# Kernel optimization log

Hardware: AMD Instinct MI355X
Metric: run time of the kernel (lower is better)

Reference implementation:

```python
import jax, jax.numpy as jnp
import numpy as np

N_NODES = 50000
N_EDGES = 800000
F_IN = 128
HID = 128  # hidden_dim * num_heads with num_heads=1
N_GRAPHS = 32
N_LAYERS = 4
NEG_SLOPE = 0.2
LN_EPS = 1e-5


def setup_inputs() -> dict:
    key = jax.random.key(0)
    ks = jax.random.split(key, 20)
    x = jax.random.normal(ks[0], (N_NODES, F_IN), dtype=jnp.float32)
    edge_index = jax.random.randint(ks[1], (2, N_EDGES), 0, N_NODES, dtype=jnp.int32)
    batch = jnp.sort(jax.random.randint(ks[2], (N_NODES,), 0, N_GRAPHS, dtype=jnp.int32))
    s = 0.05
    Ws = jax.random.normal(ks[3], (N_LAYERS, F_IN, HID), dtype=jnp.float32) * s
    a_src = jax.random.normal(ks[4], (N_LAYERS, HID), dtype=jnp.float32) * s
    a_dst = jax.random.normal(ks[5], (N_LAYERS, HID), dtype=jnp.float32) * s
    gat_b = jnp.zeros((N_LAYERS, HID), dtype=jnp.float32)
    ln_g = jnp.ones((N_LAYERS, HID), dtype=jnp.float32)
    ln_b = jnp.zeros((N_LAYERS, HID), dtype=jnp.float32)
    skip_W = jax.random.normal(ks[6], (F_IN, HID), dtype=jnp.float32) * s
    skip_b = jnp.zeros((HID,), dtype=jnp.float32)
    W1 = jax.random.normal(ks[7], (2 * HID, HID), dtype=jnp.float32) * s
    b1 = jnp.zeros((HID,), dtype=jnp.float32)
    W2 = jax.random.normal(ks[8], (HID, HID // 2), dtype=jnp.float32) * s
    b2 = jnp.zeros((HID // 2,), dtype=jnp.float32)
    W3 = jax.random.normal(ks[9], (HID // 2, 4), dtype=jnp.float32) * s
    b3 = jnp.zeros((4,), dtype=jnp.float32)
    return dict(x=x, edge_index=edge_index, batch=batch, Ws=Ws, a_src=a_src,
                a_dst=a_dst, gat_b=gat_b, ln_g=ln_g, ln_b=ln_b,
                skip_W=skip_W, skip_b=skip_b, W1=W1, b1=b1, W2=W2, b2=b2, W3=W3, b3=b3)


def _gat_layer(x, W, a_s, a_d, b, src, dst, n_nodes):
    # linear transform (single head)
    h = x @ W                                  # [N, C]
    e_src = h @ a_s                            # [N]
    e_dst = h @ a_d                            # [N]
    e = jax.nn.leaky_relu(e_src[src] + e_dst[dst], NEG_SLOPE)  # [E']
    # segment softmax over destination nodes
    m = jax.ops.segment_max(e, dst, num_segments=n_nodes)      # [N]
    p = jnp.exp(e - m[dst])
    z = jax.ops.segment_sum(p, dst, num_segments=n_nodes)      # [N]
    alpha = p / z[dst]                                         # [E']
    out = jax.ops.segment_sum(h[src] * alpha[:, None], dst, num_segments=n_nodes)
    return out + b


def _layernorm(x, g, b):
    mu = jnp.mean(x, axis=-1, keepdims=True)
    var = jnp.var(x, axis=-1, keepdims=True)
    return (x - mu) * jax.lax.rsqrt(var + LN_EPS) * g + b


def reference(x, edge_index, batch, Ws, a_src, a_dst, gat_b, ln_g, ln_b,
              skip_W, skip_b, W1, b1, W2, b2, W3, b3):
    n = x.shape[0]
    # PyG GATConv default: add self loops
    loops = jnp.arange(n, dtype=edge_index.dtype)
    src = jnp.concatenate([edge_index[0], loops])
    dst = jnp.concatenate([edge_index[1], loops])

    skip = x @ skip_W + skip_b
    h = x
    for i in range(N_LAYERS):
        h_new = _gat_layer(h, Ws[i], a_src[i], a_dst[i], gat_b[i], src, dst, n)
        h_new = _layernorm(h_new, ln_g[i], ln_b[i])
        if i < N_LAYERS - 1:
            h_new = jax.nn.elu(h_new)
        h = h_new + (skip if i == 0 else h)
    # global mean + max pool over graphs
    bidx = batch
    cnt = jax.ops.segment_sum(jnp.ones((n,), h.dtype), bidx, num_segments=N_GRAPHS)
    x_mean = jax.ops.segment_sum(h, bidx, num_segments=N_GRAPHS) / jnp.maximum(cnt, 1.0)[:, None]
    x_max = jax.ops.segment_max(h, bidx, num_segments=N_GRAPHS)
    g = jnp.concatenate([x_mean, x_max], axis=1)           # [G, 2*HID]
    g = jax.nn.relu(g @ W1 + b1)
    g = jax.nn.relu(g @ W2 + b2)
    return g @ W3 + b3
```

## Files before the change

### kernel.cpp

```cpp
#include <hip/hip_runtime.h>
#include <hip/hip_fp16.h>
#include <math.h>

#define NND 50000
#define NE  800000
#define HID 128
#define NGR 32
#define NLAYER 4
#define NPL 8
#define TOT8 (NND * NPL)
#define KSLOT 16

typedef _Float16 half8 __attribute__((ext_vector_type(8)));
typedef float float4v __attribute__((ext_vector_type(4)));

static __device__ __forceinline__ unsigned fenc(float f){
  unsigned u = __float_as_uint(f);
  return (u & 0x80000000u) ? ~u : (u | 0x80000000u);
}
static __device__ __forceinline__ float fdec(unsigned u){
  return __uint_as_float((u & 0x80000000u) ? (u & 0x7fffffffu) : ~u);
}

__global__ __launch_bounds__(256) void k_prep(const float* __restrict__ Ws, const float* __restrict__ skip_W,
    _Float16* __restrict__ wth, const int* __restrict__ ei, int* __restrict__ cnt8p,
    unsigned short* __restrict__ csrf, int E, int N)
{
  if (blockIdx.x < 5) {
    int m = blockIdx.x;
    const float* src = (m < 4) ? (Ws + (size_t)m * 16384) : skip_W;
    _Float16* oh = wth + (size_t)m * 16384;
    for (int i = threadIdx.x; i < 16384; i += 256){
      int c = i >> 7, k = i & 127;
      oh[i] = (_Float16)src[k * 128 + c];
    }
    return;
  }
  int base = (blockIdx.x - 5) * 1024 + threadIdx.x;
  int p = blockIdx.x & 7;
  int srcs[4]; int cells[4]; bool val[4];
#pragma unroll
  for (int i = 0; i < 4; ++i) {
    int e = base + i * 256;
    val[i] = e < E + N;
    int s = 0, d = 0;
    if (val[i]) {
      if (e < E) { s = ei[e]; d = ei[E + e]; } else { s = e - E; d = e - E; }
    }
    srcs[i] = s; cells[i] = p * NND + d;
  }
  int r[4];
#pragma unroll
  for (int i = 0; i < 4; ++i) r[i] = val[i] ? atomicAdd(&cnt8p[cells[i]], 1) : KSLOT;
#pragma unroll
  for (int i = 0; i < 4; ++i)
    if (r[i] < KSLOT) csrf[(size_t)cells[i] * KSLOT + r[i]] = (unsigned short)srcs[i];
}

static __device__ __forceinline__ void gemm_body(int row0, const float* __restrict__ A,
    const _Float16* __restrict__ wt, const float* __restrict__ bias,
    const float* __restrict__ a_s, const float* __restrict__ a_d,
    float* __restrict__ outF, _Float16* __restrict__ outH,
    float* __restrict__ es, float* __restrict__ ed, int N)
{
  int tid = threadIdx.x;
  int w  = tid >> 6;
  int l  = tid & 63;
  int ln = l & 15;
  int q  = l >> 4;

  int row = row0 + w * 16 + ln;
  bool rok = row < N;
  const float4* Arow = (const float4*)(A + (size_t)(rok ? row : 0) * 128);

  half8 af[4];
#pragma unroll
  for (int k32 = 0; k32 < 4; ++k32) {
    int f4 = k32 * 8 + q * 2;
    float4 a0 = make_float4(0.f,0.f,0.f,0.f), a1 = a0;
    if (rok) { a0 = Arow[f4]; a1 = Arow[f4 + 1]; }
    half8 h = {(_Float16)a0.x, (_Float16)a0.y, (_Float16)a0.z, (_Float16)a0.w,
               (_Float16)a1.x, (_Float16)a1.y, (_Float16)a1.z, (_Float16)a1.w};
    af[k32] = h;
  }

  float4v acc[8];
#pragma unroll
  for (int t = 0; t < 8; ++t) acc[t] = (float4v){0.f, 0.f, 0.f, 0.f};

#pragma unroll
  for (int k32 = 0; k32 < 4; ++k32) {
    int kk = k32 * 32 + q * 8;
#pragma unroll
    for (int t = 0; t < 8; ++t) {
      half8 bv = *(const half8*)(&wt[(size_t)(t * 16 + ln) * 128 + kk]);
      acc[t] = __builtin_amdgcn_mfma_f32_16x16x32_f16(af[k32], bv, acc[t], 0, 0, 0);
    }
  }

  float bb[8];
  if (bias) {
#pragma unroll
    for (int t = 0; t < 8; ++t) bb[t] = bias[t * 16 + ln];
  }
#pragma unroll
  for (int t = 0; t < 8; ++t) {
#pragma unroll
    for (int r = 0; r < 4; ++r) {
      int gr = row0 + w * 16 + q * 4 + r;
      if (gr < N) {
        int col = t * 16 + ln;
        float v = acc[t][r] + (bias ? bb[t] : 0.f);
        if (outF) outF[(size_t)gr * 128 + col] = v;
        if (outH) outH[(size_t)gr * 128 + col] = (_Float16)v;
      }
    }
  }
  if (a_s) {
    float asv[8], adv[8];
#pragma unroll
    for (int t = 0; t < 8; ++t) { asv[t] = a_s[t * 16 + ln]; adv[t] = a_d[t * 16 + ln]; }
    float ps[4], pd[4];
#pragma unroll
    for (int r = 0; r < 4; ++r) {
      float s_ = 0.f, d_ = 0.f;
#pragma unroll
      for (int t = 0; t < 8; ++t) { s_ += acc[t][r] * asv[t]; d_ += acc[t][r] * adv[t]; }
      ps[r] = s_; pd[r] = d_;
    }
#pragma unroll
    for (int o = 1; o < 16; o <<= 1) {
#pragma unroll
      for (int r = 0; r < 4; ++r) { ps[r] += __shfl_xor(ps[r], o); pd[r] += __shfl_xor(pd[r], o); }
    }
    if (ln == 0) {
#pragma unroll
      for (int r = 0; r < 4; ++r) {
        int gr = row0 + w * 16 + q * 4 + r;
        if (gr < N) { es[gr] = ps[r]; ed[gr] = pd[r]; }
      }
    }
  }
}

__global__ __launch_bounds__(256) void gemm_mfma(const float* __restrict__ A,
    const _Float16* __restrict__ wt, const float* __restrict__ bias,
    const float* __restrict__ a_s, const float* __restrict__ a_d,
    float* __restrict__ outF, _Float16* __restrict__ outH,
    float* __restrict__ es, float* __restrict__ ed, int N)
{
  gemm_body(blockIdx.x * 64, A, wt, bias, a_s, a_d, outF, outH, es, ed, N);
}

__global__ __launch_bounds__(256) void k_gemm0_tr(const float* __restrict__ x,
    const _Float16* __restrict__ wt, const float* __restrict__ a_s, const float* __restrict__ a_d,
    _Float16* __restrict__ hW, float* __restrict__ es, float* __restrict__ ed,
    int gblocks, const int* __restrict__ cnt8p, int* __restrict__ cnt8d, int N)
{
  if ((int)blockIdx.x < gblocks) {
    gemm_body(blockIdx.x * 64, x, wt, nullptr, a_s, a_d, nullptr, hW, es, ed, N);
    return;
  }
  int d = (blockIdx.x - gblocks) * 256 + threadIdx.x;
  if (d >= NND) return;
  int c[8];
#pragma unroll
  for (int k = 0; k < 8; ++k) c[k] = cnt8p[k * NND + d];
  ((int4*)(cnt8d + (size_t)d * NPL))[0] = make_int4(c[0], c[1], c[2], c[3]);
  ((int4*)(cnt8d + (size_t)d * NPL))[1] = make_int4(c[4], c[5], c[6], c[7]);
}

__global__ __launch_bounds__(256) void edge_agg(
    const __half* __restrict__ hW, const float* __restrict__ es, const float* __restrict__ ed,
    const int* __restrict__ cnt8d, const unsigned short* __restrict__ csrf,
    const float* __restrict__ gb, const float* __restrict__ lg, const float* __restrict__ lb,
    const float* __restrict__ resid, float* __restrict__ hout, int do_elu, int N)
{
  __shared__ uint2 s_as[4][64];
  int wid = threadIdx.x >> 6;
  int lane = threadIdx.x & 63;
  int sub = lane >> 4;
  int sl  = lane & 15;
  int dst = blockIdx.x * 4 + wid;
  if (dst >= N) return;

  uint4 cA = ((const uint4*)(cnt8d + (size_t)dst * NPL))[0];
  uint4 cB = ((const uint4*)(cnt8d + (size_t)dst * NPL))[1];
  int cntv[8] = {(int)cA.x,(int)cA.y,(int)cA.z,(int)cA.w,(int)cB.x,(int)cB.y,(int)cB.z,(int)cB.w};
  int cum[9]; cum[0] = 0;
#pragma unroll
  for (int k = 0; k < 8; ++k) cum[k + 1] = cum[k] + cntv[k];
  int deg = cum[8];
  float edv = ed[dst];

  float acc[8];
#pragma unroll
  for (int k = 0; k < 8; ++k) acc[k] = 0.f;
  const uint4* h4 = (const uint4*)hW;
  const unsigned short* cbase = csrf + (size_t)dst * KSLOT;

  if (deg <= 64) {
    int s = 0;
    if (lane < deg) {
      int p = 0;
#pragma unroll
      for (int k = 1; k < 8; ++k) if (lane >= cum[k]) p = k;
      int er = lane - cum[p]; er = er < KSLOT ? er : (KSLOT - 1);
      s = cbase[(size_t)p * (NND * KSLOT) + er];
    }
    const int PF = 4;
    uint4 qd_pre[PF];
#pragma unroll
    for (int i = 0; i < PF; ++i) {
      int idx = (i << 2) | sub;
      int sv = __shfl(s, idx);
      qd_pre[i] = make_uint4(0u, 0u, 0u, 0u);
      if (idx < deg) qd_pre[i] = h4[(size_t)sv * 16 + sl];
    }
    float x = -1e30f;
    if (lane < deg) {
      float xx = es[s] + edv;
      x = xx > 0.f ? xx : 0.2f * xx;
    }
    float m = x;
#pragma unroll
    for (int o = 32; o; o >>= 1) m = fmaxf(m, __shfl_xor(m, o));
    float p_ = (lane < deg) ? __expf(x - m) : 0.f;
    float z = p_;
#pragma unroll
    for (int o = 32; o; o >>= 1) z += __shfl_xor(z, o);
    float a_l = p_ / z;

    int iters = (deg + 3) >> 2;
#pragma unroll
    for (int i = 0; i < PF; ++i) {
      int idx = (i << 2) | sub;
      float a = __shfl(a_l, idx);
      uint4 qd = qd_pre[i];
      float2 f0 = __half22float2(*(__half2*)&qd.x);
      float2 f1 = __half22float2(*(__half2*)&qd.y);
      float2 f2 = __half22float2(*(__half2*)&qd.z);
      float2 f3 = __half22float2(*(__half2*)&qd.w);
      acc[0] += a * f0.x; acc[1] += a * f0.y;
      acc[2] += a * f1.x; acc[3] += a * f1.y;
      acc[4] += a * f2.x; acc[5] += a * f2.y;
      acc[6] += a * f3.x; acc[7] += a * f3.y;
    }
    for (int i = PF; i < iters; ++i) {
      int idx = (i << 2) | sub;
      float a = __shfl(a_l, idx);
      int sv = __shfl(s, idx);
      if (idx < deg) {
        uint4 qd = h4[(size_t)sv * 16 + sl];
        float2 f0 = __half22float2(*(__half2*)&qd.x);
        float2 f1 = __half22float2(*(__half2*)&qd.y);
        float2 f2 = __half22float2(*(__half2*)&qd.z);
        float2 f3 = __half22float2(*(__half2*)&qd.w);
        acc[0] += a * f0.x; acc[1] += a * f0.y;
        acc[2] += a * f1.x; acc[3] += a * f1.y;
        acc[4] += a * f2.x; acc[5] += a * f2.y;
        acc[6] += a * f3.x; acc[7] += a * f3.y;
      }
    }
  } else {
    float m = -1e30f;
    for (int j = lane; j < deg; j += 64) {
      int p = 0;
#pragma unroll
      for (int k = 1; k < 8; ++k) if (j >= cum[k]) p = k;
      int er = j - cum[p]; er = er < KSLOT ? er : (KSLOT - 1);
      float x = es[cbase[(size_t)p * (NND * KSLOT) + er]] + edv;
      x = x > 0.f ? x : 0.2f * x;
      m = fmaxf(m, x);
    }
#pragma unroll
    for (int o = 32; o; o >>= 1) m = fmaxf(m, __shfl_xor(m, o));
    float z = 0.f;
    for (int j = lane; j < deg; j += 64) {
      int p = 0;
#pragma unroll
      for (int k = 1; k < 8; ++k) if (j >= cum[k]) p = k;
      int er = j - cum[p]; er = er < KSLOT ? er : (KSLOT - 1);
      float x = es[cbase[(size_t)p * (NND * KSLOT) + er]] + edv;
      x = x > 0.f ? x : 0.2f * x;
      z += __expf(x - m);
    }
#pragma unroll
    for (int o = 32; o; o >>= 1) z += __shfl_xor(z, o);
    float inv_z = 1.0f / z;
    for (int c0 = 0; c0 < deg; c0 += 64) {
      int j = c0 + lane;
      int cnt = min(64, deg - c0);
      int s = 0; float p_ = 0.f;
      if (j < deg) {
        int p = 0;
#pragma unroll
        for (int k = 1; k < 8; ++k) if (j >= cum[k]) p = k;
        int er = j - cum[p]; er = er < KSLOT ? er : (KSLOT - 1);
        s = cbase[(size_t)p * (NND * KSLOT) + er];
        float x = es[s] + edv;
        x = x > 0.f ? x : 0.2f * x;
        p_ = __expf(x - m) * inv_z;
      }
      s_as[wid][lane] = make_uint2(__float_as_uint(p_), (unsigned)s);
      int iters = (cnt + 3) >> 2;
      for (int i = 0; i < iters; ++i) {
        int idx = (i << 2) | sub;
        bool valid = idx < cnt;
        uint2 av = s_as[wid][valid ? idx : 0];
        float a = valid ? __uint_as_float(av.x) : 0.f;
        uint4 qd = h4[(size_t)av.y * 16 + sl];
        float2 f0 = __half22float2(*(__half2*)&qd.x);
        float2 f1 = __half22float2(*(__half2*)&qd.y);
        float2 f2 = __half22float2(*(__half2*)&qd.z);
        float2 f3 = __half22float2(*(__half2*)&qd.w);
        acc[0] += a * f0.x; acc[1] += a * f0.y;
        acc[2] += a * f1.x; acc[3] += a * f1.y;
        acc[4] += a * f2.x; acc[5] += a * f2.y;
        acc[6] += a * f3.x; acc[7] += a * f3.y;
      }
    }
  }

#pragma unroll
  for (int k = 0; k < 8; ++k) {
    acc[k] += __shfl_xor(acc[k], 16);
    acc[k] += __shfl_xor(acc[k], 32);
  }

  float4 g0 = ((const float4*)gb)[sl * 2];
  float4 g1 = ((const float4*)gb)[sl * 2 + 1];
  float v[8];
  v[0] = acc[0] + g0.x; v[1] = acc[1] + g0.y; v[2] = acc[2] + g0.z; v[3] = acc[3] + g0.w;
  v[4] = acc[4] + g1.x; v[5] = acc[5] + g1.y; v[6] = acc[6] + g1.z; v[7] = acc[7] + g1.w;
  float s1 = 0.f, s2 = 0.f;
#pragma unroll
  for (int k = 0; k < 8; ++k) { s1 += v[k]; s2 += v[k] * v[k]; }
#pragma unroll
  for (int o = 8; o; o >>= 1) { s1 += __shfl_xor(s1, o); s2 += __shfl_xor(s2, o); }
  float mu = s1 * (1.f / 128.f);
  float var = s2 * (1.f / 128.f) - mu * mu;
  float rstd = rsqrtf(var + 1e-5f);

  float va = sub == 0 ? v[0] : (sub == 1 ? v[2] : (sub == 2 ? v[4] : v[6]));
  float vb = sub == 0 ? v[1] : (sub == 1 ? v[3] : (sub == 2 ? v[5] : v[7]));
  int col = sl * 8 + sub * 2;
  float2 Lv = *(const float2*)(lg + col);
  float2 Bv = *(const float2*)(lb + col);
  float2 Rv = *(const float2*)(resid + (long)dst * 128 + col);
  float t0 = (va - mu) * rstd * Lv.x + Bv.x;
  float t1 = (vb - mu) * rstd * Lv.y + Bv.y;
  if (do_elu) {
    t0 = t0 > 0.f ? t0 : __expf(t0) - 1.f;
    t1 = t1 > 0.f ? t1 : __expf(t1) - 1.f;
  }
  *(float2*)(hout + (long)dst * 128 + col) = make_float2(t0 + Rv.x, t1 + Rv.y);
}

__global__ __launch_bounds__(128) void k_pool(const float* __restrict__ h, const int* __restrict__ batch,
    float* __restrict__ gsum, unsigned* __restrict__ gmax, int* __restrict__ gcnt, int N)
{
  int n0 = blockIdx.x * 64;
  int c = threadIdx.x;
  int cur = -1; float ls = 0.f, lm = -1e30f; int lc = 0;
  for (int i = 0; i < 64; ++i) {
    int n = n0 + i;
    if (n >= N) break;
    int g = batch[n];
    if (g != cur) {
      if (lc > 0) {
        atomicAdd(&gsum[cur * HID + c], ls);
        atomicMax(&gmax[cur * HID + c], fenc(lm));
        if (c == 0) atomicAdd(&gcnt[cur], lc);
      }
      cur = g; ls = 0.f; lm = -1e30f; lc = 0;
    }
    float v = h[(long)n * HID + c];
    ls += v; lm = fmaxf(lm, v); lc++;
  }
  if (lc > 0) {
    atomicAdd(&gsum[cur * HID + c], ls);
    atomicMax(&gmax[cur * HID + c], fenc(lm));
    if (c == 0) atomicAdd(&gcnt[cur], lc);
  }
}

__global__ __launch_bounds__(128) void k_mlp(const float* __restrict__ gsum,
    const unsigned* __restrict__ gmax, const int* __restrict__ gcnt,
    const float* __restrict__ W1, const float* __restrict__ b1,
    const float* __restrict__ W2, const float* __restrict__ b2,
    const float* __restrict__ W3, const float* __restrict__ b3,
    float* __restrict__ out)
{
  int g = blockIdx.x;
  int c = threadIdx.x;
  __shared__ float G[256];
  __shared__ float O1[128];
  __shared__ float O2[64];
  float inv = 1.0f / fmaxf((float)gcnt[g], 1.0f);
  G[c]       = gsum[g * HID + c] * inv;
  G[128 + c] = fdec(gmax[g * HID + c]);
  __syncthreads();
  {
    float acc = 0.f;
#pragma unroll 8
    for (int k = 0; k < 256; ++k) acc += G[k] * W1[k * 128 + c];
    float v = acc + b1[c];
    O1[c] = v > 0.f ? v : 0.f;
  }
  __syncthreads();
  if (c < 64) {
    float acc = 0.f;
#pragma unroll 8
    for (int k = 0; k < 128; ++k) acc += O1[k] * W2[k * 64 + c];
    float v = acc + b2[c];
    O2[c] = v > 0.f ? v : 0.f;
  }
  __syncthreads();
  if (c < 4) {
    float acc = 0.f;
#pragma unroll 8
    for (int k = 0; k < 64; ++k) acc += O2[k] * W3[k * 4 + c];
    out[g * 4 + c] = acc + b3[c];
  }
}

extern "C" void kernel_launch(void* const* d_in, const int* in_sizes, int n_in,
                              void* d_out, int out_size, void* d_ws, size_t ws_size,
                              hipStream_t stream) {
  const float* x      = (const float*)d_in[0];
  const int*   ei     = (const int*)d_in[1];
  const int*   batch  = (const int*)d_in[2];
  const float* Ws     = (const float*)d_in[3];
  const float* a_src  = (const float*)d_in[4];
  const float* a_dst  = (const float*)d_in[5];
  const float* gat_b  = (const float*)d_in[6];
  const float* ln_g   = (const float*)d_in[7];
  const float* ln_b   = (const float*)d_in[8];
  const float* skip_W = (const float*)d_in[9];
  const float* skip_b = (const float*)d_in[10];
  const float* W1     = (const float*)d_in[11];
  const float* b1     = (const float*)d_in[12];
  const float* W2     = (const float*)d_in[13];
  const float* b2     = (const float*)d_in[14];
  const float* W3     = (const float*)d_in[15];
  const float* b3     = (const float*)d_in[16];
  float* out = (float*)d_out;

  const int N = NND, E = NE;

  char* p = (char*)d_ws;
  auto alloc = [&](size_t bytes) -> void* {
    void* r = (void*)p;
    p += (bytes + 255) & ~(size_t)255;
    return r;
  };
  float*  skip  = (float*)alloc(sizeof(float) * (size_t)N * HID);
  float*  hcur  = (float*)alloc(sizeof(float) * (size_t)N * HID);
  _Float16* hW  = (_Float16*)alloc(sizeof(_Float16) * (size_t)N * HID);
  float*  es    = (float*)alloc(sizeof(float) * N);
  float*  ed    = (float*)alloc(sizeof(float) * N);
  int*    cnt8p = (int*)alloc(sizeof(int) * TOT8);
  int*    cnt8d = (int*)alloc(sizeof(int) * TOT8);
  unsigned short* csrf = (unsigned short*)alloc(sizeof(unsigned short) * (size_t)TOT8 * KSLOT);
  _Float16* wth = (_Float16*)alloc(sizeof(_Float16) * 5 * 16384);
  char*   zbeg  = p;
  float*  gsum  = (float*)alloc(sizeof(float) * NGR * HID);
  unsigned* gmax = (unsigned*)alloc(sizeof(unsigned) * NGR * HID);
  int*    gcnt  = (int*)alloc(sizeof(int) * NGR);
  size_t zlen = (size_t)(p - zbeg);

  int gblocks = (N + 63) / 64;
  int cblocks = (E + N + 1023) / 1024;
  int tblocks = (N + 255) / 256;

  hipMemsetAsync(cnt8p, 0, sizeof(int) * TOT8, stream);
  k_prep<<<5 + cblocks, 256, 0, stream>>>(Ws, skip_W, wth, ei, cnt8p, csrf, E, N);

  gemm_mfma<<<gblocks, 256, 0, stream>>>(x, wth + 4 * 16384, skip_b, nullptr, nullptr,
                                         skip, nullptr, nullptr, nullptr, N);

  k_gemm0_tr<<<gblocks + tblocks, 256, 0, stream>>>(x, wth, a_src, a_dst, hW, es, ed,
                                                    gblocks, cnt8p, cnt8d, N);
  edge_agg<<<(N + 3) / 4, 256, 0, stream>>>((const __half*)hW, es, ed, cnt8d, csrf,
                                 gat_b, ln_g, ln_b, skip, hcur, 1, N);

  for (int l = 1; l < NLAYER; ++l) {
    gemm_mfma<<<gblocks, 256, 0, stream>>>(hcur, wth + (size_t)l * 16384, nullptr,
                                           a_src + l * HID, a_dst + l * HID,
                                           nullptr, hW, es, ed, N);
    edge_agg<<<(N + 3) / 4, 256, 0, stream>>>((const __half*)hW, es, ed, cnt8d, csrf,
                                   gat_b + l * HID, ln_g + l * HID, ln_b + l * HID,
                                   hcur, hcur, (l < NLAYER - 1) ? 1 : 0, N);
  }

  hipMemsetAsync(zbeg, 0, zlen, stream);
  k_pool<<<(N + 63) / 64, 128, 0, stream>>>(hcur, batch, gsum, gmax, gcnt, N);
  k_mlp<<<NGR, 128, 0, stream>>>(gsum, gmax, gcnt, W1, b1, W2, b2, W3, b3, out);
}
```

Baseline: 456.9 us.

## Replace slotted partitioned adjacency with exact CSR via two-level bucket sort

Builds a compact CSR (starts plus 16-bit source list) with a coarse 256-node bucket count, two prefix scans, a scatter into buckets and a per-bucket fine sort. The previous layout used 8 partitions with 16 fixed slots per destination and per-destination prefix logic. Edge aggregation now reads one contiguous source range per node, with simpler indexing and a smaller adjacency footprint. The cost is more preprocessing launches and an extra pass over the edges. The old fixed slots also silently dropped overflow edges, and the exact CSR removes that.

```diff
diff --git a/kernel.cpp b/kernel.cpp
--- a/kernel.cpp
+++ b/kernel.cpp
@@ -7,9 +7,9 @@
 #define HID 128
 #define NGR 32
 #define NLAYER 4
-#define NPL 8
-#define TOT8 (NND * NPL)
-#define KSLOT 16
+#define NBK 196
+#define NBLK 831
+#define NITEM (NE + NND)
 
 typedef _Float16 half8 __attribute__((ext_vector_type(8)));
 typedef float float4v __attribute__((ext_vector_type(4)));
@@ -22,9 +22,9 @@
   return __uint_as_float((u & 0x80000000u) ? (u & 0x7fffffffu) : ~u);
 }
 
-__global__ __launch_bounds__(256) void k_prep(const float* __restrict__ Ws, const float* __restrict__ skip_W,
-    _Float16* __restrict__ wth, const int* __restrict__ ei, int* __restrict__ cnt8p,
-    unsigned short* __restrict__ csrf, int E, int N)
+
+__global__ __launch_bounds__(256) void k_count(const float* __restrict__ Ws, const float* __restrict__ skip_W,
+    _Float16* __restrict__ wth, const int* __restrict__ ei, unsigned short* __restrict__ cnts)
 {
   if (blockIdx.x < 5) {
     int m = blockIdx.x;
@@ -36,25 +36,132 @@
     }
     return;
   }
-  int base = (blockIdx.x - 5) * 1024 + threadIdx.x;
-  int p = blockIdx.x & 7;
-  int srcs[4]; int cells[4]; bool val[4];
+  int blk = blockIdx.x - 5;
+  __shared__ unsigned h[NBK];
+  for (int i = threadIdx.x; i < NBK; i += 256) h[i] = 0;
+  __syncthreads();
+  int e0 = blk * 1024 + threadIdx.x;
 #pragma unroll
   for (int i = 0; i < 4; ++i) {
-    int e = base + i * 256;
-    val[i] = e < E + N;
-    int s = 0, d = 0;
-    if (val[i]) {
-      if (e < E) { s = ei[e]; d = ei[E + e]; } else { s = e - E; d = e - E; }
-    }
-    srcs[i] = s; cells[i] = p * NND + d;
-  }
-  int r[4];
-#pragma unroll
-  for (int i = 0; i < 4; ++i) r[i] = val[i] ? atomicAdd(&cnt8p[cells[i]], 1) : KSLOT;
-#pragma unroll
-  for (int i = 0; i < 4; ++i)
-    if (r[i] < KSLOT) csrf[(size_t)cells[i] * KSLOT + r[i]] = (unsigned short)srcs[i];
+    int e = e0 + i * 256;
+    if (e < NITEM) {
+      int d = (e < NE) ? ei[NE + e] : (e - NE);
+      atomicAdd(&h[d >> 8], 1u);
+    }
+  }
+  __syncthreads();
+  for (int i = threadIdx.x; i < NBK; i += 256)
+    cnts[(size_t)i * NBLK + blk] = (unsigned short)h[i];
+}
+
+__global__ __launch_bounds__(256) void k_scan1(const unsigned short* __restrict__ cnts,
+    unsigned* __restrict__ offs, unsigned* __restrict__ totals)
+{
+  int b = blockIdx.x;
+  int t = threadIdx.x;
+  int lane = t & 63, wid = t >> 6;
+  unsigned v[4];
+  int i0 = t * 4;
+#pragma unroll
+  for (int k = 0; k < 4; ++k) {
+    int i = i0 + k;
+    v[k] = (i < NBLK) ? (unsigned)cnts[(size_t)b * NBLK + i] : 0u;
+  }
+  unsigned cs = v[0] + v[1] + v[2] + v[3];
+  unsigned incl = cs;
+#pragma unroll
+  for (int o = 1; o < 64; o <<= 1) { unsigned u = __shfl_up(incl, o); if (lane >= o) incl += u; }
+  __shared__ unsigned wsum[4];
+  if (lane == 63) wsum[wid] = incl;
+  __syncthreads();
+  unsigned wbase = 0;
+#pragma unroll
+  for (int k = 0; k < 4; ++k) if (k < wid) wbase += wsum[k];
+  unsigned run = wbase + incl - cs;
+#pragma unroll
+  for (int k = 0; k < 4; ++k) {
+    int i = i0 + k;
+    if (i < NBLK) offs[(size_t)b * NBLK + i] = run;
+    run += v[k];
+  }
+  if (t == 255) totals[b] = wbase + incl;
+}
+
+__global__ __launch_bounds__(256) void k_scan2(const unsigned* __restrict__ totals, unsigned* __restrict__ base)
+{
+  int t = threadIdx.x;
+  int lane = t & 63, wid = t >> 6;
+  unsigned v = (t < NBK) ? totals[t] : 0u;
+  unsigned incl = v;
+#pragma unroll
+  for (int o = 1; o < 64; o <<= 1) { unsigned u = __shfl_up(incl, o); if (lane >= o) incl += u; }
+  __shared__ unsigned wsum[4];
+  if (lane == 63) wsum[wid] = incl;
+  __syncthreads();
+  unsigned wbase = 0;
+#pragma unroll
+  for (int k = 0; k < 4; ++k) if (k < wid) wbase += wsum[k];
+  if (t < NBK) base[t] = wbase + incl - v;
+  if (t == 255) base[NBK] = wbase + incl;
+}
+
+__global__ __launch_bounds__(256) void k_scatter(const int* __restrict__ ei, const unsigned* __restrict__ offs,
+    const unsigned* __restrict__ base, unsigned* __restrict__ ebuf)
+{
+  int blk = blockIdx.x;
+  __shared__ unsigned cur[NBK];
+  for (int i = threadIdx.x; i < NBK; i += 256)
+    cur[i] = base[i] + offs[(size_t)i * NBLK + blk];
+  __syncthreads();
+  int e0 = blk * 1024 + threadIdx.x;
+#pragma unroll
+  for (int i = 0; i < 4; ++i) {
+    int e = e0 + i * 256;
+    if (e < NITEM) {
+      int s, d;
+      if (e < NE) { s = ei[e]; d = ei[NE + e]; } else { s = e - NE; d = e - NE; }
+      unsigned pos = atomicAdd(&cur[d >> 8], 1u);
+      ebuf[pos] = ((unsigned)d << 16) | (unsigned)s;
+    }
+  }
+}
+
+__global__ __launch_bounds__(256) void k_fine(const unsigned* __restrict__ ebuf, const unsigned* __restrict__ base,
+    unsigned* __restrict__ starts, unsigned short* __restrict__ srcs, int N)
+{
+  int b = blockIdx.x;
+  int t = threadIdx.x;
+  unsigned lo = base[b], hi = base[b + 1];
+  int d0 = b << 8;
+  __shared__ unsigned h[256], st[256], wsum[4];
+  h[t] = 0;
+  __syncthreads();
+  for (unsigned i = lo + t; i < hi; i += 256)
+    atomicAdd(&h[(ebuf[i] >> 16) - d0], 1u);
+  __syncthreads();
+  unsigned v = h[t];
+  int lane = t & 63, wid = t >> 6;
+  unsigned incl = v;
+#pragma unroll
+  for (int o = 1; o < 64; o <<= 1) { unsigned u = __shfl_up(incl, o); if (lane >= o) incl += u; }
+  if (lane == 63) wsum[wid] = incl;
+  __syncthreads();
+  unsigned wbase = 0;
+#pragma unroll
+  for (int k = 0; k < 4; ++k) if (k < wid) wbase += wsum[k];
+  unsigned excl = wbase + incl - v;
+  st[t] = excl;
+  int dst = d0 + t;
+  if (dst < N) starts[dst] = lo + excl;
+  if (b == NBK - 1 && t == 0) starts[N] = hi;
+  h[t] = 0;
+  __syncthreads();
+  for (unsigned i = lo + t; i < hi; i += 256) {
+    unsigned w = ebuf[i];
+    unsigned dl = (w >> 16) - d0;
+    unsigned r = atomicAdd(&h[dl], 1u);
+    srcs[lo + st[dl] + r] = (unsigned short)(w & 0xFFFFu);
+  }
 }
 
 static __device__ __forceinline__ void gemm_body(int row0, const float* __restrict__ A,
@@ -152,27 +259,9 @@
   gemm_body(blockIdx.x * 64, A, wt, bias, a_s, a_d, outF, outH, es, ed, N);
 }
 
-__global__ __launch_bounds__(256) void k_gemm0_tr(const float* __restrict__ x,
-    const _Float16* __restrict__ wt, const float* __restrict__ a_s, const float* __restrict__ a_d,
-    _Float16* __restrict__ hW, float* __restrict__ es, float* __restrict__ ed,
-    int gblocks, const int* __restrict__ cnt8p, int* __restrict__ cnt8d, int N)
-{
-  if ((int)blockIdx.x < gblocks) {
-    gemm_body(blockIdx.x * 64, x, wt, nullptr, a_s, a_d, nullptr, hW, es, ed, N);
-    return;
-  }
-  int d = (blockIdx.x - gblocks) * 256 + threadIdx.x;
-  if (d >= NND) return;
-  int c[8];
-#pragma unroll
-  for (int k = 0; k < 8; ++k) c[k] = cnt8p[k * NND + d];
-  ((int4*)(cnt8d + (size_t)d * NPL))[0] = make_int4(c[0], c[1], c[2], c[3]);
-  ((int4*)(cnt8d + (size_t)d * NPL))[1] = make_int4(c[4], c[5], c[6], c[7]);
-}
-
 __global__ __launch_bounds__(256) void edge_agg(
     const __half* __restrict__ hW, const float* __restrict__ es, const float* __restrict__ ed,
-    const int* __restrict__ cnt8d, const unsigned short* __restrict__ csrf,
+    const unsigned* __restrict__ starts, const unsigned short* __restrict__ srcs,
     const float* __restrict__ gb, const float* __restrict__ lg, const float* __restrict__ lb,
     const float* __restrict__ resid, float* __restrict__ hout, int do_elu, int N)
 {
@@ -184,30 +273,18 @@
   int dst = blockIdx.x * 4 + wid;
   if (dst >= N) return;
 
-  uint4 cA = ((const uint4*)(cnt8d + (size_t)dst * NPL))[0];
-  uint4 cB = ((const uint4*)(cnt8d + (size_t)dst * NPL))[1];
-  int cntv[8] = {(int)cA.x,(int)cA.y,(int)cA.z,(int)cA.w,(int)cB.x,(int)cB.y,(int)cB.z,(int)cB.w};
-  int cum[9]; cum[0] = 0;
-#pragma unroll
-  for (int k = 0; k < 8; ++k) cum[k + 1] = cum[k] + cntv[k];
-  int deg = cum[8];
+  unsigned st0 = starts[dst];
+  int deg = (int)(starts[dst + 1] - st0);
   float edv = ed[dst];
 
   float acc[8];
 #pragma unroll
   for (int k = 0; k < 8; ++k) acc[k] = 0.f;
   const uint4* h4 = (const uint4*)hW;
-  const unsigned short* cbase = csrf + (size_t)dst * KSLOT;
 
   if (deg <= 64) {
     int s = 0;
-    if (lane < deg) {
-      int p = 0;
-#pragma unroll
-      for (int k = 1; k < 8; ++k) if (lane >= cum[k]) p = k;
-      int er = lane - cum[p]; er = er < KSLOT ? er : (KSLOT - 1);
-      s = cbase[(size_t)p * (NND * KSLOT) + er];
-    }
+    if (lane < deg) s = srcs[st0 + lane];
     const int PF = 4;
     uint4 qd_pre[PF];
 #pragma unroll
@@ -265,11 +342,7 @@
   } else {
     float m = -1e30f;
     for (int j = lane; j < deg; j += 64) {
-      int p = 0;
-#pragma unroll
-      for (int k = 1; k < 8; ++k) if (j >= cum[k]) p = k;
-      int er = j - cum[p]; er = er < KSLOT ? er : (KSLOT - 1);
-      float x = es[cbase[(size_t)p * (NND * KSLOT) + er]] + edv;
+      float x = es[srcs[st0 + j]] + edv;
       x = x > 0.f ? x : 0.2f * x;
       m = fmaxf(m, x);
     }
@@ -277,11 +350,7 @@
     for (int o = 32; o; o >>= 1) m = fmaxf(m, __shfl_xor(m, o));
     float z = 0.f;
     for (int j = lane; j < deg; j += 64) {
-      int p = 0;
-#pragma unroll
-      for (int k = 1; k < 8; ++k) if (j >= cum[k]) p = k;
-      int er = j - cum[p]; er = er < KSLOT ? er : (KSLOT - 1);
-      float x = es[cbase[(size_t)p * (NND * KSLOT) + er]] + edv;
+      float x = es[srcs[st0 + j]] + edv;
       x = x > 0.f ? x : 0.2f * x;
       z += __expf(x - m);
     }
@@ -293,11 +362,7 @@
       int cnt = min(64, deg - c0);
       int s = 0; float p_ = 0.f;
       if (j < deg) {
-        int p = 0;
-#pragma unroll
-        for (int k = 1; k < 8; ++k) if (j >= cum[k]) p = k;
-        int er = j - cum[p]; er = er < KSLOT ? er : (KSLOT - 1);
-        s = cbase[(size_t)p * (NND * KSLOT) + er];
+        s = srcs[st0 + j];
         float x = es[s] + edv;
         x = x > 0.f ? x : 0.2f * x;
         p_ = __expf(x - m) * inv_z;
@@ -447,7 +512,7 @@
   const float* b3     = (const float*)d_in[16];
   float* out = (float*)d_out;
 
-  const int N = NND, E = NE;
+  const int N = NND;
 
   char* p = (char*)d_ws;
   auto alloc = [&](size_t bytes) -> void* {
@@ -460,10 +525,14 @@
   _Float16* hW  = (_Float16*)alloc(sizeof(_Float16) * (size_t)N * HID);
   float*  es    = (float*)alloc(sizeof(float) * N);
   float*  ed    = (float*)alloc(sizeof(float) * N);
-  int*    cnt8p = (int*)alloc(sizeof(int) * TOT8);
-  int*    cnt8d = (int*)alloc(sizeof(int) * TOT8);
-  unsigned short* csrf = (unsigned short*)alloc(sizeof(unsigned short) * (size_t)TOT8 * KSLOT);
   _Float16* wth = (_Float16*)alloc(sizeof(_Float16) * 5 * 16384);
+  unsigned short* cnts = (unsigned short*)alloc(sizeof(unsigned short) * (size_t)NBK * NBLK);
+  unsigned* offs   = (unsigned*)alloc(sizeof(unsigned) * (size_t)NBK * NBLK);
+  unsigned* totals = (unsigned*)alloc(sizeof(unsigned) * NBK);
+  unsigned* base   = (unsigned*)alloc(sizeof(unsigned) * (NBK + 1));
+  unsigned* ebuf   = (unsigned*)alloc(sizeof(unsigned) * (size_t)NITEM);
+  unsigned* starts = (unsigned*)alloc(sizeof(unsigned) * (N + 1));
+  unsigned short* srcs = (unsigned short*)alloc(sizeof(unsigned short) * (size_t)NITEM);
   char*   zbeg  = p;
   float*  gsum  = (float*)alloc(sizeof(float) * NGR * HID);
   unsigned* gmax = (unsigned*)alloc(sizeof(unsigned) * NGR * HID);
@@ -471,25 +540,26 @@
   size_t zlen = (size_t)(p - zbeg);
 
   int gblocks = (N + 63) / 64;
-  int cblocks = (E + N + 1023) / 1024;
-  int tblocks = (N + 255) / 256;
-
-  hipMemsetAsync(cnt8p, 0, sizeof(int) * TOT8, stream);
-  k_prep<<<5 + cblocks, 256, 0, stream>>>(Ws, skip_W, wth, ei, cnt8p, csrf, E, N);
+
+  k_count  <<<5 + NBLK, 256, 0, stream>>>(Ws, skip_W, wth, ei, cnts);
+  k_scan1  <<<NBK, 256, 0, stream>>>(cnts, offs, totals);
+  k_scan2  <<<1, 256, 0, stream>>>(totals, base);
+  k_scatter<<<NBLK, 256, 0, stream>>>(ei, offs, base, ebuf);
+  k_fine   <<<NBK, 256, 0, stream>>>(ebuf, base, starts, srcs, N);
 
   gemm_mfma<<<gblocks, 256, 0, stream>>>(x, wth + 4 * 16384, skip_b, nullptr, nullptr,
                                          skip, nullptr, nullptr, nullptr, N);
 
-  k_gemm0_tr<<<gblocks + tblocks, 256, 0, stream>>>(x, wth, a_src, a_dst, hW, es, ed,
-                                                    gblocks, cnt8p, cnt8d, N);
-  edge_agg<<<(N + 3) / 4, 256, 0, stream>>>((const __half*)hW, es, ed, cnt8d, csrf,
+  gemm_mfma<<<gblocks, 256, 0, stream>>>(x, wth, nullptr, a_src, a_dst,
+                                         nullptr, hW, es, ed, N);
+  edge_agg<<<(N + 3) / 4, 256, 0, stream>>>((const __half*)hW, es, ed, starts, srcs,
                                  gat_b, ln_g, ln_b, skip, hcur, 1, N);
 
   for (int l = 1; l < NLAYER; ++l) {
     gemm_mfma<<<gblocks, 256, 0, stream>>>(hcur, wth + (size_t)l * 16384, nullptr,
                                            a_src + l * HID, a_dst + l * HID,
                                            nullptr, hW, es, ed, N);
-    edge_agg<<<(N + 3) / 4, 256, 0, stream>>>((const __half*)hW, es, ed, cnt8d, csrf,
+    edge_agg<<<(N + 3) / 4, 256, 0, stream>>>((const __half*)hW, es, ed, starts, srcs,
                                    gat_b + l * HID, ln_g + l * HID, ln_b + l * HID,
                                    hcur, hcur, (l < NLAYER - 1) ? 1 : 0, N);
   }
```

Result: faster. 444.0 us (-2.8%).
